# Kernel tuning notes

Measured on AMD Instinct MI355X. Metric: run time of the kernel, lower is better.

The kernel has to match this reference:

```python
import jax, jax.numpy as jnp
import numpy as np

DIMS = 2048
HEADS = 16
HEAD_DIM = DIMS // HEADS  # 128
WIN = 256
THETA = 10000.0


def rotate_half(x):
    x1, x2 = jnp.split(x, 2, axis=-1)
    return jnp.concatenate([-x2, x1], axis=-1)


def rope_freqs(seq_len):
    inv_freq = 1.0 / (THETA ** (jnp.arange(0, HEAD_DIM, 2, dtype=jnp.float32) / HEAD_DIM))
    f = jnp.outer(jnp.arange(seq_len, dtype=jnp.float32), inv_freq)  # [S, D/2]
    return jnp.concatenate([f, f], axis=-1)[None, :, None, :]  # [1, S, 1, D]


def setup_inputs() -> dict:
    key = jax.random.key(0)
    ks = jax.random.split(key, 5)
    B, S = 2, 8192
    scale = 1.0 / np.sqrt(DIMS).astype(np.float32)
    return {
        "hidden_states": jax.random.normal(ks[0], (B, S, DIMS), jnp.float32),
        "Wq": jax.random.normal(ks[1], (DIMS, DIMS), jnp.float32) * scale,
        "Wk": jax.random.normal(ks[2], (DIMS, DIMS), jnp.float32) * scale,
        "Wv": jax.random.normal(ks[3], (DIMS, DIMS), jnp.float32) * scale,
        "Wo": jax.random.normal(ks[4], (DIMS, DIMS), jnp.float32) * scale,
    }


def reference(hidden_states, Wq, Wk, Wv, Wo):
    B, S, _ = hidden_states.shape
    # projections (weights stored [in, out])
    q = (hidden_states @ Wq).reshape(B, S, HEADS, HEAD_DIM)
    k = (hidden_states @ Wk).reshape(B, S, HEADS, HEAD_DIM)
    v = (hidden_states @ Wv).reshape(B, S, HEADS, HEAD_DIM)

    freqs = rope_freqs(S)
    cos, sin = jnp.cos(freqs), jnp.sin(freqs)
    q = q * cos + rotate_half(q) * sin
    k = k * cos + rotate_half(k) * sin

    C = S // WIN
    qc = q.reshape(B, C, WIN, HEADS, HEAD_DIM)
    kc = k.reshape(B, C, WIN, HEADS, HEAD_DIM)
    vc = v.reshape(B, C, WIN, HEADS, HEAD_DIM)

    # previous chunk's K/V (zeros for chunk 0; masked out anyway)
    kp = jnp.concatenate([jnp.zeros_like(kc[:, :1]), kc[:, :-1]], axis=1)
    vp = jnp.concatenate([jnp.zeros_like(vc[:, :1]), vc[:, :-1]], axis=1)
    kcat = jnp.concatenate([kp, kc], axis=2)  # [B, C, 2W, H, D]
    vcat = jnp.concatenate([vp, vc], axis=2)

    scores = jnp.einsum('bcqhd,bckhd->bchqk', qc, kcat) / np.float32(np.sqrt(HEAD_DIM))

    causal = jnp.tril(jnp.ones((WIN, WIN), dtype=bool))  # current-chunk causal
    prev_ok = (jnp.arange(C) > 0)[:, None, None]  # chunk 0 has no previous chunk
    mask = jnp.concatenate([
        jnp.broadcast_to(prev_ok, (C, WIN, WIN)),
        jnp.broadcast_to(causal[None], (C, WIN, WIN)),
    ], axis=-1)  # [C, W, 2W]

    scores = jnp.where(mask[None, :, None], scores, -jnp.inf)
    probs = jax.nn.softmax(scores, axis=-1)
    out = jnp.einsum('bchqk,bckhd->bcqhd', probs, vcat)
    out = out.reshape(B, S, DIMS)
    return out @ Wo
```

## Files before the change

### kernel.cpp

```cpp
#include <hip/hip_runtime.h>
#include <cmath>

#define DIMS 2048
#define SEQ  8192
#define NB   2
#define HEADS 16
#define HD   128
#define WINW 256
#define MROWS 16384
#define NCH  32

using bf16x8 = __attribute__((ext_vector_type(8))) short;
using f32x4  = __attribute__((ext_vector_type(4))) float;

__device__ __forceinline__ unsigned short f2bf(float f) {
  unsigned int u = __float_as_uint(f);
  u += 0x7FFF + ((u >> 16) & 1);
  return (unsigned short)(u >> 16);
}

__device__ __forceinline__ void async16(const unsigned short* g, unsigned short* l) {
  __builtin_amdgcn_global_load_lds((const __attribute__((address_space(1))) void*)g,
                                   (__attribute__((address_space(3))) void*)l,
                                   16, 0, 0);
}

#define BAR() __builtin_amdgcn_s_barrier()
#define WAIT_LGKM0() do { asm volatile("s_waitcnt lgkmcnt(0)" ::: "memory"); \
                          __builtin_amdgcn_sched_barrier(0); } while (0)
#define WAIT_VM(n) asm volatile("s_waitcnt vmcnt(" #n ")" ::: "memory")
#define MFMA16(a, b, c) __builtin_amdgcn_mfma_f32_16x16x32_bf16(a, b, c, 0, 0, 0)

__global__ void wconv(const float* __restrict__ w0, const float* __restrict__ w1,
                      const float* __restrict__ w2, const float* __restrict__ w3,
                      unsigned short* __restrict__ Wt) {
  __shared__ unsigned short tile[64][65];
  const float* W = (blockIdx.z == 0) ? w0 : (blockIdx.z == 1) ? w1 : (blockIdx.z == 2) ? w2 : w3;
  unsigned short* O = Wt + (size_t)blockIdx.z * DIMS * DIMS;
  const int k0 = blockIdx.y * 64, n0 = blockIdx.x * 64;
  const int t = threadIdx.x;
  #pragma unroll
  for (int p = 0; p < 16; ++p) {
    int i = p * 4 + (t >> 6);
    int j = t & 63;
    tile[i][j] = f2bf(W[(size_t)(k0 + i) * DIMS + n0 + j]);
  }
  __syncthreads();
  #pragma unroll
  for (int p = 0; p < 16; ++p) {
    int a = p * 4 + (t >> 6);
    int b = t & 63;
    O[(size_t)(n0 + a) * DIMS + k0 + b] = tile[b][a];
  }
}

__global__ void hconv(const float* __restrict__ in, unsigned short* __restrict__ outp) {
  const long n4 = (long)MROWS * DIMS / 4;
  long i = (long)blockIdx.x * blockDim.x + threadIdx.x;
  const long stride = (long)gridDim.x * blockDim.x;
  for (; i < n4; i += stride) {
    float4 v = ((const float4*)in)[i];
    ushort4 o;
    o.x = f2bf(v.x); o.y = f2bf(v.y); o.z = f2bf(v.z); o.w = f2bf(v.w);
    ((ushort4*)outp)[i] = o;
  }
}

__global__ void rope_tab(float* __restrict__ cosT, float* __restrict__ sinT) {
  int t = blockIdx.x * 256 + threadIdx.x;
  int pos = t >> 6, i = t & 63;
  double inv = pow(10000.0, -(double)i / 64.0);
  double ang = (double)pos * inv;
  cosT[t] = (float)cos(ang);
  sinT[t] = (float)sin(ang);
}

template<int MODE>
__global__ __launch_bounds__(512, 2) void gemm256(
    const unsigned short* __restrict__ A,
    const unsigned short* __restrict__ WtAll,
    unsigned short* __restrict__ OutB,
    float* __restrict__ OutF,
    const float* __restrict__ cosT,
    const float* __restrict__ sinT) {
  __shared__ __align__(1024) unsigned short lds[65536];
  unsigned short* const As0 = lds;
  unsigned short* const Bs0 = lds + 16384;
  unsigned short* const As1 = lds + 32768;
  unsigned short* const Bs1 = lds + 49152;

  const int tid = threadIdx.x;
  const int wid = tid >> 6, lane = tid & 63;
  const int lo = lane & 15, hi = lane >> 4;
  const int wm = wid >> 2, wn = wid & 3;
  const int flip = (lo & 7) << 4;

  const int nwg = gridDim.x;
  const int orig = blockIdx.x;
  const int bid = (orig & 7) * (nwg >> 3) + (orig >> 3);

  int by, bx, z;
  if (MODE == 0) {
    z = bid >> 9;
    by = (bid & 511) >> 3;
    bx = bid & 7;
  } else {
    by = bid >> 3; bx = bid & 7; z = 3;
  }
  const int m0 = by * 256, n0 = bx * 256;
  const unsigned short* const Ag = A;
  const unsigned short* const Bg = WtAll + (size_t)z * DIMS * DIMS;

  f32x4 acc[8][4];
  #pragma unroll
  for (int i = 0; i < 8; ++i)
    #pragma unroll
    for (int j = 0; j < 4; ++j)
      acc[i][j] = (f32x4){0.f, 0.f, 0.f, 0.f};

  auto stage_half = [&](const unsigned short* __restrict__ G, int grow0, int tile,
                        unsigned short* dst) {
    const int k0 = tile * 64;
    #pragma unroll
    for (int h8 = 0; h8 < 2; ++h8) {
      const int c = h8 * 8 + wid;
      const int row = c * 8 + (lane >> 3);
      const int col8 = (lane & 7) ^ (lane >> 3);
      async16(G + (size_t)(grow0 + row) * DIMS + k0 + col8 * 8, dst + c * 512);
    }
  };
  auto rdA = [&](const unsigned short* base, int i, int kk) -> bf16x8 {
    const int r = i * 32 + wm * 16 + lo;
    const int cb = (kk * 64 + hi * 16) ^ flip;
    return *(const bf16x8*)((const char*)base + r * 128 + cb);
  };
  auto rdB = [&](const unsigned short* base, int j, int kk) -> bf16x8 {
    const int r = j * 64 + wn * 16 + lo;
    const int cb = (kk * 64 + hi * 16) ^ flip;
    return *(const bf16x8*)((const char*)base + r * 128 + cb);
  };

  bf16x8 aq[4][2], b0[2][2], b1[2][2];

  stage_half(Ag, m0,       0, As0);
  stage_half(Bg, n0,       0, Bs0);
  stage_half(Ag, m0 + 128, 0, As0 + 8192);
  stage_half(Bg, n0 + 128, 0, Bs0 + 8192);
  stage_half(Ag, m0,       1, As1);
  stage_half(Bg, n0,       1, Bs1);
  stage_half(Bg, n0 + 128, 1, Bs1 + 8192);
  WAIT_VM(6);
  BAR();

  #pragma unroll 1
  for (int it = 0; it < 16; ++it) {
    const int t = 2 * it;
    const bool pre = (it < 15);
    #pragma unroll
    for (int i = 0; i < 4; ++i) { aq[i][0] = rdA(As0, i, 0); aq[i][1] = rdA(As0, i, 1); }
    #pragma unroll
    for (int j = 0; j < 2; ++j) { b0[j][0] = rdB(Bs0, j, 0); b0[j][1] = rdB(Bs0, j, 1); }
    stage_half(Ag, m0 + 128, t + 1, As1 + 8192);
    WAIT_LGKM0();
    __builtin_amdgcn_s_setprio(1);
    #pragma unroll
    for (int kk = 0; kk < 2; ++kk)
      #pragma unroll
      for (int i = 0; i < 4; ++i)
        #pragma unroll
        for (int j = 0; j < 2; ++j)
          acc[i][j] = MFMA16(aq[i][kk], b0[j][kk], acc[i][j]);
    __builtin_amdgcn_s_setprio(0);
    BAR();
    #pragma unroll
    for (int j = 0; j < 2; ++j) { b1[j][0] = rdB(Bs0, 2 + j, 0); b1[j][1] = rdB(Bs0, 2 + j, 1); }
    if (pre) stage_half(Ag, m0, t + 2, As0);
    WAIT_LGKM0();
    __builtin_amdgcn_s_setprio(1);
    #pragma unroll
    for (int kk = 0; kk < 2; ++kk)
      #pragma unroll
      for (int i = 0; i < 4; ++i)
        #pragma unroll
        for (int j = 0; j < 2; ++j)
          acc[i][2 + j] = MFMA16(aq[i][kk], b1[j][kk], acc[i][2 + j]);
    __builtin_amdgcn_s_setprio(0);
    BAR();
    #pragma unroll
    for (int i = 0; i < 4; ++i) { aq[i][0] = rdA(As0, 4 + i, 0); aq[i][1] = rdA(As0, 4 + i, 1); }
    if (pre) stage_half(Bg, n0, t + 2, Bs0);
    WAIT_LGKM0();
    __builtin_amdgcn_s_setprio(1);
    #pragma unroll
    for (int kk = 0; kk < 2; ++kk)
      #pragma unroll
      for (int i = 0; i < 4; ++i)
        #pragma unroll
        for (int j = 0; j < 2; ++j)
          acc[4 + i][j] = MFMA16(aq[i][kk], b0[j][kk], acc[4 + i][j]);
    __builtin_amdgcn_s_setprio(0);
    BAR();
    if (pre) stage_half(Bg, n0 + 128, t + 2, Bs0 + 8192);
    __builtin_amdgcn_s_setprio(1);
    #pragma unroll
    for (int kk = 0; kk < 2; ++kk)
      #pragma unroll
      for (int i = 0; i < 4; ++i)
        #pragma unroll
        for (int j = 0; j < 2; ++j)
          acc[4 + i][2 + j] = MFMA16(aq[i][kk], b1[j][kk], acc[4 + i][2 + j]);
    __builtin_amdgcn_s_setprio(0);
    if (it == 15) { WAIT_VM(0); } else { WAIT_VM(6); }
    BAR();
    #pragma unroll
    for (int i = 0; i < 4; ++i) { aq[i][0] = rdA(As1, i, 0); aq[i][1] = rdA(As1, i, 1); }
    #pragma unroll
    for (int j = 0; j < 2; ++j) { b0[j][0] = rdB(Bs1, j, 0); b0[j][1] = rdB(Bs1, j, 1); }
    if (pre) stage_half(Ag, m0 + 128, t + 2, As0 + 8192);
    WAIT_LGKM0();
    __builtin_amdgcn_s_setprio(1);
    #pragma unroll
    for (int kk = 0; kk < 2; ++kk)
      #pragma unroll
      for (int i = 0; i < 4; ++i)
        #pragma unroll
        for (int j = 0; j < 2; ++j)
          acc[i][j] = MFMA16(aq[i][kk], b0[j][kk], acc[i][j]);
    __builtin_amdgcn_s_setprio(0);
    BAR();
    #pragma unroll
    for (int j = 0; j < 2; ++j) { b1[j][0] = rdB(Bs1, 2 + j, 0); b1[j][1] = rdB(Bs1, 2 + j, 1); }
    if (pre) stage_half(Ag, m0, t + 3, As1);
    WAIT_LGKM0();
    __builtin_amdgcn_s_setprio(1);
    #pragma unroll
    for (int kk = 0; kk < 2; ++kk)
      #pragma unroll
      for (int i = 0; i < 4; ++i)
        #pragma unroll
        for (int j = 0; j < 2; ++j)
          acc[i][2 + j] = MFMA16(aq[i][kk], b1[j][kk], acc[i][2 + j]);
    __builtin_amdgcn_s_setprio(0);
    BAR();
    #pragma unroll
    for (int i = 0; i < 4; ++i) { aq[i][0] = rdA(As1, 4 + i, 0); aq[i][1] = rdA(As1, 4 + i, 1); }
    if (pre) stage_half(Bg, n0, t + 3, Bs1);
    WAIT_LGKM0();
    __builtin_amdgcn_s_setprio(1);
    #pragma unroll
    for (int kk = 0; kk < 2; ++kk)
      #pragma unroll
      for (int i = 0; i < 4; ++i)
        #pragma unroll
        for (int j = 0; j < 2; ++j)
          acc[4 + i][j] = MFMA16(aq[i][kk], b0[j][kk], acc[4 + i][j]);
    __builtin_amdgcn_s_setprio(0);
    BAR();
    if (pre) stage_half(Bg, n0 + 128, t + 3, Bs1 + 8192);
    __builtin_amdgcn_s_setprio(1);
    #pragma unroll
    for (int kk = 0; kk < 2; ++kk)
      #pragma unroll
      for (int i = 0; i < 4; ++i)
        #pragma unroll
        for (int j = 0; j < 2; ++j)
          acc[4 + i][2 + j] = MFMA16(aq[i][kk], b1[j][kk], acc[4 + i][2 + j]);
    __builtin_amdgcn_s_setprio(0);
    WAIT_VM(6);
    BAR();
  }

  if (MODE == 0 && z == 2) {
    unsigned short* vt = OutB + (size_t)2 * MROWS * DIMS;
    #pragma unroll
    for (int i = 0; i < 8; ++i) {
      const int row0 = m0 + i * 32 + wm * 16 + hi * 4;
      const int bb = row0 >> 13;
      const int s0 = row0 & (SEQ - 1);
      #pragma unroll
      for (int j = 0; j < 4; ++j) {
        const int colg = n0 + j * 64 + wn * 16 + lo;
        ushort4 pk;
        pk.x = f2bf(acc[i][j][0]); pk.y = f2bf(acc[i][j][1]);
        pk.z = f2bf(acc[i][j][2]); pk.w = f2bf(acc[i][j][3]);
        *(ushort4*)&vt[(((size_t)(bb * 2048 + colg)) << 13) + s0] = pk;
      }
    }
  } else {
    unsigned short* outb = (MODE == 0) ? (OutB + (size_t)z * MROWS * DIMS)
                                       : (unsigned short*)nullptr;
    #pragma unroll
    for (int i = 0; i < 8; ++i) {
      #pragma unroll
      for (int rr = 0; rr < 4; ++rr) {
        const int row = m0 + i * 32 + wm * 16 + hi * 4 + rr;
        const int s = row & (SEQ - 1);
        if (MODE == 1) {
          float* o = OutF + (size_t)row * DIMS + n0;
          #pragma unroll
          for (int j = 0; j < 4; ++j) o[j * 64 + wn * 16 + lo] = acc[i][j][rr];
        } else {
          unsigned short* o = outb + (size_t)row * DIMS + n0;
          const int d = wn * 16 + lo;
          const float cc = cosT[s * 64 + d], sn = sinT[s * 64 + d];
          #pragma unroll
          for (int p = 0; p < 2; ++p) {
            const float v1 = acc[i][2 * p][rr], v2 = acc[i][2 * p + 1][rr];
            o[p * 128 + d]      = f2bf(v1 * cc - v2 * sn);
            o[p * 128 + d + 64] = f2bf(v2 * cc + v1 * sn);
          }
        }
      }
    }
  }
}

__global__ __launch_bounds__(512) void attn(
    const unsigned short* __restrict__ Qb,
    const unsigned short* __restrict__ Kb,
    const unsigned short* __restrict__ Vt,
    unsigned short* __restrict__ AO) {
  __shared__ unsigned short Ksm[2][64 * 128];
  __shared__ unsigned short Vsm[2][128 * 64];
  __shared__ unsigned short Psm[8 * 32 * 72];

  const int bid = blockIdx.x;
  const int h = bid & 15;
  const int c = (bid >> 4) & 31;
  const int b = bid >> 9;
  const int tid = threadIdx.x;
  const int wid = tid >> 6, lane = tid & 63;
  const int lo = lane & 15, hi = lane >> 4;
  const float SCALE = 0.08838834764831845f;

  bf16x8 qf[2][4];
  {
    const size_t base = ((size_t)(b * SEQ + c * WINW + wid * 32 + lo)) * DIMS + h * HD;
    #pragma unroll
    for (int m = 0; m < 2; ++m)
      #pragma unroll
      for (int ks = 0; ks < 4; ++ks)
        qf[m][ks] = *(const bf16x8*)&Qb[base + (size_t)m * 16 * DIMS + ks * 32 + hi * 8];
  }

  f32x4 O[2][8];
  float mrow[2][4], lrow[2][4];
  #pragma unroll
  for (int m = 0; m < 2; ++m) {
    #pragma unroll
    for (int n = 0; n < 8; ++n) O[m][n] = (f32x4){0.f, 0.f, 0.f, 0.f};
    #pragma unroll
    for (int r = 0; r < 4; ++r) { mrow[m][r] = -INFINITY; lrow[m][r] = 0.f; }
  }

  unsigned short* Pw = Psm + wid * 32 * 72;
  const int t0 = (c == 0) ? 4 : 0;

  const unsigned short* Kg0 = Kb + ((size_t)(b * SEQ + (c - 1) * WINW)) * DIMS + h * HD;
  const unsigned short* Vg0 = Vt + (((size_t)(b * 2048 + h * HD)) << 13) + (c - 1) * WINW;

  auto stageKV = [&](int t, int pb) {
    #pragma unroll
    for (int p = 0; p < 2; ++p) {
      const int cid = p * 512 + tid;
      const int row = cid >> 4, c16 = cid & 15;
      async16(Kg0 + (size_t)(t * 64 + row) * DIMS + ((c16 ^ (row & 7)) << 3),
              &Ksm[pb][cid * 8]);
    }
    #pragma unroll
    for (int p = 0; p < 2; ++p) {
      const int cid = p * 512 + tid;
      const int rd = cid >> 3, c8 = cid & 7;
      async16(Vg0 + ((size_t)rd << 13) + t * 64 + ((c8 ^ (rd & 7)) << 3),
              &Vsm[pb][cid * 8]);
    }
  };

  stageKV(t0, t0 & 1);
  for (int t = t0; t < 8; ++t) {
    const int pb = t & 1;
    if (t < 7) { stageKV(t + 1, pb ^ 1); WAIT_VM(4); } else { WAIT_VM(0); }
    BAR();

    f32x4 S[2][4];
    #pragma unroll
    for (int m = 0; m < 2; ++m)
      #pragma unroll
      for (int n = 0; n < 4; ++n)
        S[m][n] = (f32x4){0.f, 0.f, 0.f, 0.f};
    const char* Kbase = (const char*)&Ksm[pb][0];
    #pragma unroll
    for (int ks = 0; ks < 4; ++ks) {
      bf16x8 kf[4];
      #pragma unroll
      for (int n = 0; n < 4; ++n)
        kf[n] = *(const bf16x8*)(Kbase + (n * 16 + lo) * 256 +
                                 (((ks * 4 + hi) ^ (lo & 7)) << 4));
      #pragma unroll
      for (int m = 0; m < 2; ++m)
        #pragma unroll
        for (int n = 0; n < 4; ++n)
          S[m][n] = MFMA16(qf[m][ks], kf[n], S[m][n]);
    }

    float tmax[2][4];
    #pragma unroll
    for (int m = 0; m < 2; ++m) {
      #pragma unroll
      for (int r = 0; r < 4; ++r) {
        const int qrow = wid * 32 + m * 16 + hi * 4 + r;
        float tm = -INFINITY;
        #pragma unroll
        for (int n = 0; n < 4; ++n) {
          const int kc = t * 64 + n * 16 + lo;
          float v = S[m][n][r] * SCALE;
          const bool ok = (kc < WINW) ? (c > 0) : ((kc - WINW) <= qrow);
          v = ok ? v : -INFINITY;
          S[m][n][r] = v;
          tm = fmaxf(tm, v);
        }
        tm = fmaxf(tm, __shfl_xor(tm, 1));
        tm = fmaxf(tm, __shfl_xor(tm, 2));
        tm = fmaxf(tm, __shfl_xor(tm, 4));
        tm = fmaxf(tm, __shfl_xor(tm, 8));
        tmax[m][r] = tm;
      }
    }
    float need = -INFINITY;
    #pragma unroll
    for (int m = 0; m < 2; ++m)
      #pragma unroll
      for (int r = 0; r < 4; ++r)
        need = fmaxf(need, tmax[m][r] - mrow[m][r]);
    const bool fast = __all(need <= 8.0f);

    #pragma unroll
    for (int m = 0; m < 2; ++m) {
      #pragma unroll
      for (int r = 0; r < 4; ++r) {
        float mused = mrow[m][r];
        if (!fast) {
          mused = fmaxf(mused, tmax[m][r]);
          const float corr = __expf(mrow[m][r] - mused);
          lrow[m][r] *= corr;
          #pragma unroll
          for (int n = 0; n < 8; ++n) O[m][n][r] *= corr;
          mrow[m][r] = mused;
        }
        float rsum = 0.f;
        #pragma unroll
        for (int n = 0; n < 4; ++n) {
          const float p = __expf(S[m][n][r] - mused);
          S[m][n][r] = p;
          rsum += p;
        }
        rsum += __shfl_xor(rsum, 1);
        rsum += __shfl_xor(rsum, 2);
        rsum += __shfl_xor(rsum, 4);
        rsum += __shfl_xor(rsum, 8);
        lrow[m][r] += rsum;
        #pragma unroll
        for (int n = 0; n < 4; ++n)
          Pw[(m * 16 + hi * 4 + r) * 72 + n * 16 + lo] = f2bf(S[m][n][r]);
      }
    }
    asm volatile("" ::: "memory");

    const char* Vbase = (const char*)&Vsm[pb][0];
    #pragma unroll
    for (int kk = 0; kk < 2; ++kk) {
      const int ko = kk * 32 + hi * 8;
      bf16x8 pf[2], vf[8];
      #pragma unroll
      for (int m = 0; m < 2; ++m)
        pf[m] = *(const bf16x8*)&Pw[(m * 16 + lo) * 72 + ko];
      #pragma unroll
      for (int n = 0; n < 8; ++n)
        vf[n] = *(const bf16x8*)(Vbase + (n * 16 + lo) * 128 +
                                 (((kk * 4 + hi) ^ (lo & 7)) << 4));
      #pragma unroll
      for (int m = 0; m < 2; ++m)
        #pragma unroll
        for (int n = 0; n < 8; ++n)
          O[m][n] = MFMA16(pf[m], vf[n], O[m][n]);
    }
    BAR();
  }

  #pragma unroll
  for (int m = 0; m < 2; ++m) {
    #pragma unroll
    for (int r = 0; r < 4; ++r) {
      const float inv = 1.f / lrow[m][r];
      const size_t row = (size_t)(b * SEQ + c * WINW + wid * 32 + m * 16 + hi * 4 + r);
      unsigned short* o = AO + row * DIMS + h * HD;
      #pragma unroll
      for (int n = 0; n < 8; ++n)
        o[n * 16 + lo] = f2bf(O[m][n][r] * inv);
    }
  }
}

extern "C" void kernel_launch(void* const* d_in, const int* in_sizes, int n_in,
                              void* d_out, int out_size, void* d_ws, size_t ws_size,
                              hipStream_t stream) {
  const float* H  = (const float*)d_in[0];
  const float* Wq = (const float*)d_in[1];
  const float* Wk = (const float*)d_in[2];
  const float* Wv = (const float*)d_in[3];
  const float* Wo = (const float*)d_in[4];
  float* out = (float*)d_out;

  unsigned short* Wt  = (unsigned short*)d_ws;
  unsigned short* Hb  = Wt + (size_t)4 * DIMS * DIMS;
  unsigned short* QKV = Hb + (size_t)MROWS * DIMS;
  unsigned short* AO  = QKV + (size_t)3 * MROWS * DIMS;
  float* cosT = (float*)(AO + (size_t)MROWS * DIMS);
  float* sinT = cosT + (size_t)SEQ * 64;

  wconv<<<dim3(32, 32, 4), 256, 0, stream>>>(Wq, Wk, Wv, Wo, Wt);
  hconv<<<2048, 256, 0, stream>>>(H, Hb);
  rope_tab<<<2048, 256, 0, stream>>>(cosT, sinT);
  gemm256<0><<<1536, 512, 0, stream>>>(Hb, Wt, QKV, nullptr, cosT, sinT);
  attn<<<dim3(1024), 512, 0, stream>>>(QKV, QKV + (size_t)MROWS * DIMS,
                                       QKV + (size_t)2 * MROWS * DIMS, AO);
  gemm256<1><<<512, 512, 0, stream>>>(AO, Wt, nullptr, out, cosT, sinT);
}
```

Baseline: 714.6 us.

## Load full LDS tile fragments up front and merge four MFMA phases into one

Each half-iteration of the GEMM main loop now reads all A and B fragments for the k-tile from LDS at once. It then issues one barrier, stages the next tiles' global-to-LDS loads together, and runs all 32 MFMAs in a single block. Previously the loop had four phases, each with its own barrier and interleaved staging. This drops three barriers per half-iteration and gives the scheduler longer MFMA runs. The cost is more live registers for the extra fragment arrays, and the global loads are issued in one burst instead of spread across the phases.

```diff
diff --git a/kernel.cpp b/kernel.cpp
--- a/kernel.cpp
+++ b/kernel.cpp
@@ -140,7 +140,7 @@
     return *(const bf16x8*)((const char*)base + r * 128 + cb);
   };
 
-  bf16x8 aq[4][2], b0[2][2], b1[2][2];
+  bf16x8 aq0[4][2], aq1[4][2], b0[2][2], b1[2][2];
 
   stage_half(Ag, m0,       0, As0);
   stage_half(Bg, n0,       0, Bs0);
@@ -156,115 +156,71 @@
   for (int it = 0; it < 16; ++it) {
     const int t = 2 * it;
     const bool pre = (it < 15);
-    #pragma unroll
-    for (int i = 0; i < 4; ++i) { aq[i][0] = rdA(As0, i, 0); aq[i][1] = rdA(As0, i, 1); }
-    #pragma unroll
-    for (int j = 0; j < 2; ++j) { b0[j][0] = rdB(Bs0, j, 0); b0[j][1] = rdB(Bs0, j, 1); }
+
+    #pragma unroll
+    for (int i = 0; i < 4; ++i) {
+      aq0[i][0] = rdA(As0, i, 0);     aq0[i][1] = rdA(As0, i, 1);
+      aq1[i][0] = rdA(As0, 4 + i, 0); aq1[i][1] = rdA(As0, 4 + i, 1);
+    }
+    #pragma unroll
+    for (int j = 0; j < 2; ++j) {
+      b0[j][0] = rdB(Bs0, j, 0);     b0[j][1] = rdB(Bs0, j, 1);
+      b1[j][0] = rdB(Bs0, 2 + j, 0); b1[j][1] = rdB(Bs0, 2 + j, 1);
+    }
     stage_half(Ag, m0 + 128, t + 1, As1 + 8192);
     WAIT_LGKM0();
+    BAR();
+    if (pre) {
+      stage_half(Ag, m0,       t + 2, As0);
+      stage_half(Bg, n0,       t + 2, Bs0);
+      stage_half(Bg, n0 + 128, t + 2, Bs0 + 8192);
+    }
     __builtin_amdgcn_s_setprio(1);
     #pragma unroll
     for (int kk = 0; kk < 2; ++kk)
       #pragma unroll
       for (int i = 0; i < 4; ++i)
         #pragma unroll
-        for (int j = 0; j < 2; ++j)
-          acc[i][j] = MFMA16(aq[i][kk], b0[j][kk], acc[i][j]);
-    __builtin_amdgcn_s_setprio(0);
-    BAR();
-    #pragma unroll
-    for (int j = 0; j < 2; ++j) { b1[j][0] = rdB(Bs0, 2 + j, 0); b1[j][1] = rdB(Bs0, 2 + j, 1); }
-    if (pre) stage_half(Ag, m0, t + 2, As0);
-    WAIT_LGKM0();
-    __builtin_amdgcn_s_setprio(1);
-    #pragma unroll
-    for (int kk = 0; kk < 2; ++kk)
-      #pragma unroll
-      for (int i = 0; i < 4; ++i)
-        #pragma unroll
-        for (int j = 0; j < 2; ++j)
-          acc[i][2 + j] = MFMA16(aq[i][kk], b1[j][kk], acc[i][2 + j]);
-    __builtin_amdgcn_s_setprio(0);
-    BAR();
-    #pragma unroll
-    for (int i = 0; i < 4; ++i) { aq[i][0] = rdA(As0, 4 + i, 0); aq[i][1] = rdA(As0, 4 + i, 1); }
-    if (pre) stage_half(Bg, n0, t + 2, Bs0);
-    WAIT_LGKM0();
-    __builtin_amdgcn_s_setprio(1);
-    #pragma unroll
-    for (int kk = 0; kk < 2; ++kk)
-      #pragma unroll
-      for (int i = 0; i < 4; ++i)
-        #pragma unroll
-        for (int j = 0; j < 2; ++j)
-          acc[4 + i][j] = MFMA16(aq[i][kk], b0[j][kk], acc[4 + i][j]);
-    __builtin_amdgcn_s_setprio(0);
-    BAR();
-    if (pre) stage_half(Bg, n0 + 128, t + 2, Bs0 + 8192);
-    __builtin_amdgcn_s_setprio(1);
-    #pragma unroll
-    for (int kk = 0; kk < 2; ++kk)
-      #pragma unroll
-      for (int i = 0; i < 4; ++i)
-        #pragma unroll
-        for (int j = 0; j < 2; ++j)
-          acc[4 + i][2 + j] = MFMA16(aq[i][kk], b1[j][kk], acc[4 + i][2 + j]);
+        for (int j = 0; j < 2; ++j) {
+          acc[i][j]         = MFMA16(aq0[i][kk], b0[j][kk], acc[i][j]);
+          acc[i][2 + j]     = MFMA16(aq0[i][kk], b1[j][kk], acc[i][2 + j]);
+          acc[4 + i][j]     = MFMA16(aq1[i][kk], b0[j][kk], acc[4 + i][j]);
+          acc[4 + i][2 + j] = MFMA16(aq1[i][kk], b1[j][kk], acc[4 + i][2 + j]);
+        }
     __builtin_amdgcn_s_setprio(0);
     if (it == 15) { WAIT_VM(0); } else { WAIT_VM(6); }
     BAR();
-    #pragma unroll
-    for (int i = 0; i < 4; ++i) { aq[i][0] = rdA(As1, i, 0); aq[i][1] = rdA(As1, i, 1); }
-    #pragma unroll
-    for (int j = 0; j < 2; ++j) { b0[j][0] = rdB(Bs1, j, 0); b0[j][1] = rdB(Bs1, j, 1); }
+
+    #pragma unroll
+    for (int i = 0; i < 4; ++i) {
+      aq0[i][0] = rdA(As1, i, 0);     aq0[i][1] = rdA(As1, i, 1);
+      aq1[i][0] = rdA(As1, 4 + i, 0); aq1[i][1] = rdA(As1, 4 + i, 1);
+    }
+    #pragma unroll
+    for (int j = 0; j < 2; ++j) {
+      b0[j][0] = rdB(Bs1, j, 0);     b0[j][1] = rdB(Bs1, j, 1);
+      b1[j][0] = rdB(Bs1, 2 + j, 0); b1[j][1] = rdB(Bs1, 2 + j, 1);
+    }
     if (pre) stage_half(Ag, m0 + 128, t + 2, As0 + 8192);
     WAIT_LGKM0();
+    BAR();
+    if (pre) {
+      stage_half(Ag, m0,       t + 3, As1);
+      stage_half(Bg, n0,       t + 3, Bs1);
+      stage_half(Bg, n0 + 128, t + 3, Bs1 + 8192);
+    }
     __builtin_amdgcn_s_setprio(1);
     #pragma unroll
     for (int kk = 0; kk < 2; ++kk)
       #pragma unroll
       for (int i = 0; i < 4; ++i)
         #pragma unroll
-        for (int j = 0; j < 2; ++j)
-          acc[i][j] = MFMA16(aq[i][kk], b0[j][kk], acc[i][j]);
-    __builtin_amdgcn_s_setprio(0);
-    BAR();
-    #pragma unroll
-    for (int j = 0; j < 2; ++j) { b1[j][0] = rdB(Bs1, 2 + j, 0); b1[j][1] = rdB(Bs1, 2 + j, 1); }
-    if (pre) stage_half(Ag, m0, t + 3, As1);
-    WAIT_LGKM0();
-    __builtin_amdgcn_s_setprio(1);
-    #pragma unroll
-    for (int kk = 0; kk < 2; ++kk)
-      #pragma unroll
-      for (int i = 0; i < 4; ++i)
-        #pragma unroll
-        for (int j = 0; j < 2; ++j)
-          acc[i][2 + j] = MFMA16(aq[i][kk], b1[j][kk], acc[i][2 + j]);
-    __builtin_amdgcn_s_setprio(0);
-    BAR();
-    #pragma unroll
-    for (int i = 0; i < 4; ++i) { aq[i][0] = rdA(As1, 4 + i, 0); aq[i][1] = rdA(As1, 4 + i, 1); }
-    if (pre) stage_half(Bg, n0, t + 3, Bs1);
-    WAIT_LGKM0();
-    __builtin_amdgcn_s_setprio(1);
-    #pragma unroll
-    for (int kk = 0; kk < 2; ++kk)
-      #pragma unroll
-      for (int i = 0; i < 4; ++i)
-        #pragma unroll
-        for (int j = 0; j < 2; ++j)
-          acc[4 + i][j] = MFMA16(aq[i][kk], b0[j][kk], acc[4 + i][j]);
-    __builtin_amdgcn_s_setprio(0);
-    BAR();
-    if (pre) stage_half(Bg, n0 + 128, t + 3, Bs1 + 8192);
-    __builtin_amdgcn_s_setprio(1);
-    #pragma unroll
-    for (int kk = 0; kk < 2; ++kk)
-      #pragma unroll
-      for (int i = 0; i < 4; ++i)
-        #pragma unroll
-        for (int j = 0; j < 2; ++j)
-          acc[4 + i][2 + j] = MFMA16(aq[i][kk], b1[j][kk], acc[4 + i][2 + j]);
+        for (int j = 0; j < 2; ++j) {
+          acc[i][j]         = MFMA16(aq0[i][kk], b0[j][kk], acc[i][j]);
+          acc[i][2 + j]     = MFMA16(aq0[i][kk], b1[j][kk], acc[i][2 + j]);
+          acc[4 + i][j]     = MFMA16(aq1[i][kk], b0[j][kk], acc[4 + i][j]);
+          acc[4 + i][2 + j] = MFMA16(aq1[i][kk], b1[j][kk], acc[4 + i][2 + j]);
+        }
     __builtin_amdgcn_s_setprio(0);
     WAIT_VM(6);
     BAR();
```

New measurement: 1.891 ms. +164.6%, slower.

## Split attention into 64-row query blocks with causal tile skipping; fuse prep kernels

Applied to the files above, without the earlier changes.

The attention kernel now runs one 256-thread workgroup per 64-query block instead of one 512-thread workgroup per 256-query chunk. Each block stops at the last key tile its causal mask allows, so fully masked current-chunk tiles are no longer loaded or computed. The softmax switches to exp2 with the log2e factor folded into the scale, and the workgroup index is remapped so neighbouring workgroups are spread out. The three preprocessing kernels are merged into one launch to save launch overhead. In exchange, the previous chunk's K/V tiles are now fetched once per query block instead of once per chunk, which adds redundant memory traffic.

```diff
diff --git a/kernel.cpp b/kernel.cpp
--- a/kernel.cpp
+++ b/kernel.cpp
@@ -31,48 +31,51 @@
 #define WAIT_VM(n) asm volatile("s_waitcnt vmcnt(" #n ")" ::: "memory")
 #define MFMA16(a, b, c) __builtin_amdgcn_mfma_f32_16x16x32_bf16(a, b, c, 0, 0, 0)
 
-__global__ void wconv(const float* __restrict__ w0, const float* __restrict__ w1,
-                      const float* __restrict__ w2, const float* __restrict__ w3,
-                      unsigned short* __restrict__ Wt) {
+__global__ __launch_bounds__(256) void prep(
+    const float* __restrict__ w0, const float* __restrict__ w1,
+    const float* __restrict__ w2, const float* __restrict__ w3,
+    const float* __restrict__ H,
+    unsigned short* __restrict__ Wt, unsigned short* __restrict__ Hb,
+    float* __restrict__ cosT, float* __restrict__ sinT) {
   __shared__ unsigned short tile[64][65];
-  const float* W = (blockIdx.z == 0) ? w0 : (blockIdx.z == 1) ? w1 : (blockIdx.z == 2) ? w2 : w3;
-  unsigned short* O = Wt + (size_t)blockIdx.z * DIMS * DIMS;
-  const int k0 = blockIdx.y * 64, n0 = blockIdx.x * 64;
+  const int bid = blockIdx.x;
   const int t = threadIdx.x;
-  #pragma unroll
-  for (int p = 0; p < 16; ++p) {
-    int i = p * 4 + (t >> 6);
-    int j = t & 63;
-    tile[i][j] = f2bf(W[(size_t)(k0 + i) * DIMS + n0 + j]);
-  }
-  __syncthreads();
-  #pragma unroll
-  for (int p = 0; p < 16; ++p) {
-    int a = p * 4 + (t >> 6);
-    int b = t & 63;
-    O[(size_t)(n0 + a) * DIMS + k0 + b] = tile[b][a];
-  }
-}
-
-__global__ void hconv(const float* __restrict__ in, unsigned short* __restrict__ outp) {
-  const long n4 = (long)MROWS * DIMS / 4;
-  long i = (long)blockIdx.x * blockDim.x + threadIdx.x;
-  const long stride = (long)gridDim.x * blockDim.x;
-  for (; i < n4; i += stride) {
-    float4 v = ((const float4*)in)[i];
-    ushort4 o;
-    o.x = f2bf(v.x); o.y = f2bf(v.y); o.z = f2bf(v.z); o.w = f2bf(v.w);
-    ((ushort4*)outp)[i] = o;
-  }
-}
-
-__global__ void rope_tab(float* __restrict__ cosT, float* __restrict__ sinT) {
-  int t = blockIdx.x * 256 + threadIdx.x;
-  int pos = t >> 6, i = t & 63;
-  double inv = pow(10000.0, -(double)i / 64.0);
-  double ang = (double)pos * inv;
-  cosT[t] = (float)cos(ang);
-  sinT[t] = (float)sin(ang);
+  if (bid < 4096) {
+    const int z = bid & 3;
+    const int rest = bid >> 2;
+    const int n0 = (rest & 31) * 64, k0 = (rest >> 5) * 64;
+    const float* W = (z == 0) ? w0 : (z == 1) ? w1 : (z == 2) ? w2 : w3;
+    unsigned short* O = Wt + (size_t)z * DIMS * DIMS;
+    #pragma unroll
+    for (int p = 0; p < 16; ++p) {
+      int i = p * 4 + (t >> 6);
+      int j = t & 63;
+      tile[i][j] = f2bf(W[(size_t)(k0 + i) * DIMS + n0 + j]);
+    }
+    __syncthreads();
+    #pragma unroll
+    for (int p = 0; p < 16; ++p) {
+      int a = p * 4 + (t >> 6);
+      int b = t & 63;
+      O[(size_t)(n0 + a) * DIMS + k0 + b] = tile[b][a];
+    }
+  } else if (bid < 6144) {
+    const long n4 = (long)MROWS * DIMS / 4;
+    long i = (long)(bid - 4096) * 256 + t;
+    for (; i < n4; i += 524288) {
+      float4 v = ((const float4*)H)[i];
+      ushort4 o;
+      o.x = f2bf(v.x); o.y = f2bf(v.y); o.z = f2bf(v.z); o.w = f2bf(v.w);
+      ((ushort4*)Hb)[i] = o;
+    }
+  } else {
+    int tl = (bid - 6144) * 256 + t;
+    int pos = tl >> 6, i = tl & 63;
+    double inv = pow(10000.0, -(double)i / 64.0);
+    double ang = (double)pos * inv;
+    cosT[tl] = (float)cos(ang);
+    sinT[tl] = (float)sin(ang);
+  }
 }
 
 template<int MODE>
@@ -315,61 +318,63 @@
   }
 }
 
-__global__ __launch_bounds__(512) void attn(
+__global__ __launch_bounds__(256, 2) void attn(
     const unsigned short* __restrict__ Qb,
     const unsigned short* __restrict__ Kb,
     const unsigned short* __restrict__ Vt,
     unsigned short* __restrict__ AO) {
   __shared__ unsigned short Ksm[2][64 * 128];
   __shared__ unsigned short Vsm[2][128 * 64];
-  __shared__ unsigned short Psm[8 * 32 * 72];
-
-  const int bid = blockIdx.x;
-  const int h = bid & 15;
-  const int c = (bid >> 4) & 31;
-  const int b = bid >> 9;
+  __shared__ unsigned short Psm[4 * 16 * 72];
+
+  const int nwg = gridDim.x;
+  const int orig = blockIdx.x;
+  const int bid = (orig & 7) * (nwg >> 3) + (orig >> 3);
+
+  const int qb = bid & 3;
+  const int h = (bid >> 2) & 15;
+  const int c = (bid >> 6) & 31;
+  const int b = bid >> 11;
   const int tid = threadIdx.x;
   const int wid = tid >> 6, lane = tid & 63;
   const int lo = lane & 15, hi = lane >> 4;
-  const float SCALE = 0.08838834764831845f;
-
-  bf16x8 qf[2][4];
+  const float K1 = 0.08838834764831845f * 1.44269504089f;
+
+  const int q0 = c * WINW + qb * 64 + wid * 16;
+
+  bf16x8 qf[4];
   {
-    const size_t base = ((size_t)(b * SEQ + c * WINW + wid * 32 + lo)) * DIMS + h * HD;
-    #pragma unroll
-    for (int m = 0; m < 2; ++m)
-      #pragma unroll
-      for (int ks = 0; ks < 4; ++ks)
-        qf[m][ks] = *(const bf16x8*)&Qb[base + (size_t)m * 16 * DIMS + ks * 32 + hi * 8];
-  }
-
-  f32x4 O[2][8];
-  float mrow[2][4], lrow[2][4];
+    const size_t base = ((size_t)(b * SEQ + q0 + lo)) * DIMS + h * HD;
+    #pragma unroll
+    for (int ks = 0; ks < 4; ++ks)
+      qf[ks] = *(const bf16x8*)&Qb[base + ks * 32 + hi * 8];
+  }
+
+  f32x4 O[8];
+  float mrow[4], lrow[4];
   #pragma unroll
-  for (int m = 0; m < 2; ++m) {
-    #pragma unroll
-    for (int n = 0; n < 8; ++n) O[m][n] = (f32x4){0.f, 0.f, 0.f, 0.f};
-    #pragma unroll
-    for (int r = 0; r < 4; ++r) { mrow[m][r] = -INFINITY; lrow[m][r] = 0.f; }
-  }
-
-  unsigned short* Pw = Psm + wid * 32 * 72;
+  for (int n = 0; n < 8; ++n) O[n] = (f32x4){0.f, 0.f, 0.f, 0.f};
+  #pragma unroll
+  for (int r = 0; r < 4; ++r) { mrow[r] = -INFINITY; lrow[r] = 0.f; }
+
+  unsigned short* Pw = Psm + wid * 16 * 72;
   const int t0 = (c == 0) ? 4 : 0;
+  const int tend = 4 + qb;
 
   const unsigned short* Kg0 = Kb + ((size_t)(b * SEQ + (c - 1) * WINW)) * DIMS + h * HD;
   const unsigned short* Vg0 = Vt + (((size_t)(b * 2048 + h * HD)) << 13) + (c - 1) * WINW;
 
   auto stageKV = [&](int t, int pb) {
     #pragma unroll
-    for (int p = 0; p < 2; ++p) {
-      const int cid = p * 512 + tid;
+    for (int p = 0; p < 4; ++p) {
+      const int cid = p * 256 + tid;
       const int row = cid >> 4, c16 = cid & 15;
       async16(Kg0 + (size_t)(t * 64 + row) * DIMS + ((c16 ^ (row & 7)) << 3),
               &Ksm[pb][cid * 8]);
     }
     #pragma unroll
-    for (int p = 0; p < 2; ++p) {
-      const int cid = p * 512 + tid;
+    for (int p = 0; p < 4; ++p) {
+      const int cid = p * 256 + tid;
       const int rd = cid >> 3, c8 = cid & 7;
       async16(Vg0 + ((size_t)rd << 13) + t * 64 + ((c8 ^ (rd & 7)) << 3),
               &Vsm[pb][cid * 8]);
@@ -377,17 +382,14 @@
   };
 
   stageKV(t0, t0 & 1);
-  for (int t = t0; t < 8; ++t) {
+  for (int t = t0; t <= tend; ++t) {
     const int pb = t & 1;
-    if (t < 7) { stageKV(t + 1, pb ^ 1); WAIT_VM(4); } else { WAIT_VM(0); }
-    BAR();
-
-    f32x4 S[2][4];
-    #pragma unroll
-    for (int m = 0; m < 2; ++m)
-      #pragma unroll
-      for (int n = 0; n < 4; ++n)
-        S[m][n] = (f32x4){0.f, 0.f, 0.f, 0.f};
+    if (t < tend) { stageKV(t + 1, pb ^ 1); WAIT_VM(8); } else { WAIT_VM(0); }
+    BAR();
+
+    f32x4 S[4];
+    #pragma unroll
+    for (int n = 0; n < 4; ++n) S[n] = (f32x4){0.f, 0.f, 0.f, 0.f};
     const char* Kbase = (const char*)&Ksm[pb][0];
     #pragma unroll
     for (int ks = 0; ks < 4; ++ks) {
@@ -397,72 +399,61 @@
         kf[n] = *(const bf16x8*)(Kbase + (n * 16 + lo) * 256 +
                                  (((ks * 4 + hi) ^ (lo & 7)) << 4));
       #pragma unroll
-      for (int m = 0; m < 2; ++m)
-        #pragma unroll
-        for (int n = 0; n < 4; ++n)
-          S[m][n] = MFMA16(qf[m][ks], kf[n], S[m][n]);
-    }
-
-    float tmax[2][4];
-    #pragma unroll
-    for (int m = 0; m < 2; ++m) {
-      #pragma unroll
-      for (int r = 0; r < 4; ++r) {
-        const int qrow = wid * 32 + m * 16 + hi * 4 + r;
-        float tm = -INFINITY;
-        #pragma unroll
-        for (int n = 0; n < 4; ++n) {
-          const int kc = t * 64 + n * 16 + lo;
-          float v = S[m][n][r] * SCALE;
-          const bool ok = (kc < WINW) ? (c > 0) : ((kc - WINW) <= qrow);
-          v = ok ? v : -INFINITY;
-          S[m][n][r] = v;
-          tm = fmaxf(tm, v);
-        }
-        tm = fmaxf(tm, __shfl_xor(tm, 1));
-        tm = fmaxf(tm, __shfl_xor(tm, 2));
-        tm = fmaxf(tm, __shfl_xor(tm, 4));
-        tm = fmaxf(tm, __shfl_xor(tm, 8));
-        tmax[m][r] = tm;
+      for (int n = 0; n < 4; ++n)
+        S[n] = MFMA16(qf[ks], kf[n], S[n]);
+    }
+
+    float tmax[4];
+    #pragma unroll
+    for (int r = 0; r < 4; ++r) {
+      const int qrow = qb * 64 + wid * 16 + hi * 4 + r;
+      float tm = -INFINITY;
+      #pragma unroll
+      for (int n = 0; n < 4; ++n) {
+        const int kc = t * 64 + n * 16 + lo;
+        float v = S[n][r] * K1;
+        const bool ok = (kc < WINW) ? (c > 0) : ((kc - WINW) <= qrow);
+        v = ok ? v : -INFINITY;
+        S[n][r] = v;
+        tm = fmaxf(tm, v);
       }
+      tm = fmaxf(tm, __shfl_xor(tm, 1));
+      tm = fmaxf(tm, __shfl_xor(tm, 2));
+      tm = fmaxf(tm, __shfl_xor(tm, 4));
+      tm = fmaxf(tm, __shfl_xor(tm, 8));
+      tmax[r] = tm;
     }
     float need = -INFINITY;
     #pragma unroll
-    for (int m = 0; m < 2; ++m)
-      #pragma unroll
-      for (int r = 0; r < 4; ++r)
-        need = fmaxf(need, tmax[m][r] - mrow[m][r]);
-    const bool fast = __all(need <= 8.0f);
-
-    #pragma unroll
-    for (int m = 0; m < 2; ++m) {
-      #pragma unroll
-      for (int r = 0; r < 4; ++r) {
-        float mused = mrow[m][r];
-        if (!fast) {
-          mused = fmaxf(mused, tmax[m][r]);
-          const float corr = __expf(mrow[m][r] - mused);
-          lrow[m][r] *= corr;
-          #pragma unroll
-          for (int n = 0; n < 8; ++n) O[m][n][r] *= corr;
-          mrow[m][r] = mused;
-        }
-        float rsum = 0.f;
-        #pragma unroll
-        for (int n = 0; n < 4; ++n) {
-          const float p = __expf(S[m][n][r] - mused);
-          S[m][n][r] = p;
-          rsum += p;
-        }
-        rsum += __shfl_xor(rsum, 1);
-        rsum += __shfl_xor(rsum, 2);
-        rsum += __shfl_xor(rsum, 4);
-        rsum += __shfl_xor(rsum, 8);
-        lrow[m][r] += rsum;
-        #pragma unroll
-        for (int n = 0; n < 4; ++n)
-          Pw[(m * 16 + hi * 4 + r) * 72 + n * 16 + lo] = f2bf(S[m][n][r]);
+    for (int r = 0; r < 4; ++r) need = fmaxf(need, tmax[r] - mrow[r]);
+    const bool fast = __all(need <= 11.54f);
+
+    #pragma unroll
+    for (int r = 0; r < 4; ++r) {
+      float mused = mrow[r];
+      if (!fast) {
+        mused = fmaxf(mused, tmax[r]);
+        const float corr = exp2f(mrow[r] - mused);
+        lrow[r] *= corr;
+        #pragma unroll
+        for (int n = 0; n < 8; ++n) O[n][r] *= corr;
+        mrow[r] = mused;
       }
+      float rsum = 0.f;
+      #pragma unroll
+      for (int n = 0; n < 4; ++n) {
+        const float p = exp2f(S[n][r] - mused);
+        S[n][r] = p;
+        rsum += p;
+      }
+      rsum += __shfl_xor(rsum, 1);
+      rsum += __shfl_xor(rsum, 2);
+      rsum += __shfl_xor(rsum, 4);
+      rsum += __shfl_xor(rsum, 8);
+      lrow[r] += rsum;
+      #pragma unroll
+      for (int n = 0; n < 4; ++n)
+        Pw[(hi * 4 + r) * 72 + n * 16 + lo] = f2bf(S[n][r]);
     }
     asm volatile("" ::: "memory");
 
@@ -470,34 +461,27 @@
     #pragma unroll
     for (int kk = 0; kk < 2; ++kk) {
       const int ko = kk * 32 + hi * 8;
-      bf16x8 pf[2], vf[8];
-      #pragma unroll
-      for (int m = 0; m < 2; ++m)
-        pf[m] = *(const bf16x8*)&Pw[(m * 16 + lo) * 72 + ko];
+      bf16x8 pf = *(const bf16x8*)&Pw[lo * 72 + ko];
+      bf16x8 vf[8];
       #pragma unroll
       for (int n = 0; n < 8; ++n)
         vf[n] = *(const bf16x8*)(Vbase + (n * 16 + lo) * 128 +
                                  (((kk * 4 + hi) ^ (lo & 7)) << 4));
       #pragma unroll
-      for (int m = 0; m < 2; ++m)
-        #pragma unroll
-        for (int n = 0; n < 8; ++n)
-          O[m][n] = MFMA16(pf[m], vf[n], O[m][n]);
+      for (int n = 0; n < 8; ++n)
+        O[n] = MFMA16(pf, vf[n], O[n]);
     }
     BAR();
   }
 
   #pragma unroll
-  for (int m = 0; m < 2; ++m) {
-    #pragma unroll
-    for (int r = 0; r < 4; ++r) {
-      const float inv = 1.f / lrow[m][r];
-      const size_t row = (size_t)(b * SEQ + c * WINW + wid * 32 + m * 16 + hi * 4 + r);
-      unsigned short* o = AO + row * DIMS + h * HD;
-      #pragma unroll
-      for (int n = 0; n < 8; ++n)
-        o[n * 16 + lo] = f2bf(O[m][n][r] * inv);
-    }
+  for (int r = 0; r < 4; ++r) {
+    const float inv = 1.f / lrow[r];
+    const size_t row = (size_t)(b * SEQ + q0 + hi * 4 + r);
+    unsigned short* o = AO + row * DIMS + h * HD;
+    #pragma unroll
+    for (int n = 0; n < 8; ++n)
+      o[n * 16 + lo] = f2bf(O[n][r] * inv);
   }
 }
 
@@ -518,11 +502,9 @@
   float* cosT = (float*)(AO + (size_t)MROWS * DIMS);
   float* sinT = cosT + (size_t)SEQ * 64;
 
-  wconv<<<dim3(32, 32, 4), 256, 0, stream>>>(Wq, Wk, Wv, Wo, Wt);
-  hconv<<<2048, 256, 0, stream>>>(H, Hb);
-  rope_tab<<<2048, 256, 0, stream>>>(cosT, sinT);
+  prep<<<8192, 256, 0, stream>>>(Wq, Wk, Wv, Wo, H, Wt, Hb, cosT, sinT);
   gemm256<0><<<1536, 512, 0, stream>>>(Hb, Wt, QKV, nullptr, cosT, sinT);
-  attn<<<dim3(1024), 512, 0, stream>>>(QKV, QKV + (size_t)MROWS * DIMS,
-                                       QKV + (size_t)2 * MROWS * DIMS, AO);
+  attn<<<4096, 256, 0, stream>>>(QKV, QKV + (size_t)MROWS * DIMS,
+                                 QKV + (size_t)2 * MROWS * DIMS, AO);
   gemm256<1><<<512, 512, 0, stream>>>(AO, Wt, nullptr, out, cosT, sinT);
 }
```

Result: slower. 760.6 us (+6.4%).
